# Kernel tuning notes

Measured on AMD Instinct MI355X. Metric: run time of the kernel, lower is better.

The kernel has to match this reference:

```python
import jax, jax.numpy as jnp
import numpy as np

N = 100000   # nodes
E = 1600000  # edges
F = 128      # in_feats
H = 4        # heads
D = 32       # out_feats per head
NEG_SLOPE = 0.2


def setup_inputs() -> dict:
    key = jax.random.key(0)
    k1, k2, k3, k4, k5, k6 = jax.random.split(key, 6)
    feat = jax.random.normal(k1, (N, F), dtype=jnp.float32)
    W = jax.random.normal(k2, (H * D, F), dtype=jnp.float32) * (1.0 / np.sqrt(F))
    attn_l = jax.random.normal(k3, (1, H, D), dtype=jnp.float32) * 0.1
    attn_r = jax.random.normal(k4, (1, H, D), dtype=jnp.float32) * 0.1
    src = jax.random.randint(k5, (E,), 0, N, dtype=jnp.int32)
    dst = jax.random.randint(k6, (E,), 0, N, dtype=jnp.int32)
    return {"feat": feat, "W": W, "attn_l": attn_l, "attn_r": attn_r, "src": src, "dst": dst}


def reference(feat, W, attn_l, attn_r, src, dst):
    # fc projection: [N, F] -> [N, H, D]
    h = (feat @ W.T).reshape(N, H, D)
    # per-node attention logits [N, H]
    el = jnp.sum(h * attn_l, axis=-1)
    er = jnp.sum(h * attn_r, axis=-1)
    # edge scores: el[src] + er[dst] -> leaky relu  [E, H]
    e = jax.nn.leaky_relu(el[src] + er[dst], negative_slope=NEG_SLOPE)
    # segment softmax over edges grouped by destination node, per head
    m = jax.ops.segment_max(e, dst, num_segments=N)          # [N, H]
    ex = jnp.exp(e - m[dst])                                 # [E, H]
    s = jax.ops.segment_sum(ex, dst, num_segments=N)         # [N, H]
    alpha = ex / s[dst]                                      # [E, H]
    # weighted sparse aggregation: out[dst] += alpha * h[src]
    msgs = alpha[:, :, None] * h[src]                        # [E, H, D]
    rst = jax.ops.segment_sum(msgs, dst, num_segments=N)     # [N, H, D]
    return rst
```

## Files before the change

### kernel.cpp

```cpp
#include <hip/hip_runtime.h>

constexpr int N_NODES = 100000;
constexpr int E_EDGES = 1600000;
constexpr int NBLK    = (N_NODES + 1023) / 1024;
constexpr int GEMM_BLOCKS = (N_NODES + 63) / 64;
constexpr int HIST_BLOCKS = (E_EDGES / 4 + 255) / 256;

typedef _Float16 f16;
typedef _Float16 f16x2 __attribute__((ext_vector_type(2)));
typedef _Float16 f16x8 __attribute__((ext_vector_type(8)));
typedef float f32x4 __attribute__((ext_vector_type(4)));

__global__ __launch_bounds__(256, 2) void k_gemm_hist(
        const float* __restrict__ feat, const float* __restrict__ W,
        const float* __restrict__ attn_l, const float* __restrict__ attn_r,
        f16* __restrict__ h2, float* __restrict__ el, float* __restrict__ er,
        const int4* __restrict__ dst4, int* __restrict__ deg,
        int4* __restrict__ rank4) {
    __shared__ f16 Wlds[128 * 128];

    if (blockIdx.x >= GEMM_BLOCKS) {
        int t = (blockIdx.x - GEMM_BLOCKS) * 256 + threadIdx.x;
        if (t < E_EDGES / 4) {
            int4 d = dst4[t];
            int r0 = atomicAdd(&deg[d.x], 1);
            int r1 = atomicAdd(&deg[d.y], 1);
            int r2 = atomicAdd(&deg[d.z], 1);
            int r3 = atomicAdd(&deg[d.w], 1);
            rank4[t] = make_int4(r0, r1, r2, r3);
        }
        return;
    }

    char* wb = (char*)Wlds;
    const int tid = threadIdx.x;
    {
        int n = tid >> 1;
        int kh = (tid & 1) * 64;
        const float* wsrc = W + n * 128 + kh;
#pragma unroll
        for (int q = 0; q < 8; ++q) {
            float4 u0 = *reinterpret_cast<const float4*>(wsrc + q * 8);
            float4 u1 = *reinterpret_cast<const float4*>(wsrc + q * 8 + 4);
            f16x8 v;
            v[0] = (f16)u0.x; v[1] = (f16)u0.y; v[2] = (f16)u0.z; v[3] = (f16)u0.w;
            v[4] = (f16)u1.x; v[5] = (f16)u1.y; v[6] = (f16)u1.z; v[7] = (f16)u1.w;
            unsigned byte = (unsigned)(n * 256 + kh * 2 + q * 16) ^ ((n & 7) << 4);
            *reinterpret_cast<f16x8*>(wb + byte) = v;
        }
    }
    __syncthreads();

    const int wav  = tid >> 6;
    const int lane = tid & 63;
    const int la = lane & 15;
    const int lb = lane >> 4;
    const int row0w = blockIdx.x * 64 + wav * 16;

    f16x8 afrag[4];
    {
        int rowA = row0w + la;
        if (rowA >= N_NODES) rowA = N_NODES - 1;
        const float* ap = feat + (size_t)rowA * 128 + lb * 8;
#pragma unroll
        for (int kk = 0; kk < 4; ++kk) {
            float4 u0 = *reinterpret_cast<const float4*>(ap + kk * 32);
            float4 u1 = *reinterpret_cast<const float4*>(ap + kk * 32 + 4);
            f16x8 a;
            a[0] = (f16)u0.x; a[1] = (f16)u0.y; a[2] = (f16)u0.z; a[3] = (f16)u0.w;
            a[4] = (f16)u1.x; a[5] = (f16)u1.y; a[6] = (f16)u1.z; a[7] = (f16)u1.w;
            afrag[kk] = a;
        }
    }

    f32x4 acc[8];
#pragma unroll
    for (int t = 0; t < 8; ++t) acc[t] = (f32x4){0.f, 0.f, 0.f, 0.f};

#pragma unroll
    for (int t = 0; t < 8; ++t) {
        int col = t * 16 + la;
#pragma unroll
        for (int kk = 0; kk < 4; ++kk) {
            unsigned byte = (unsigned)(col * 256 + (kk * 32 + lb * 8) * 2) ^ ((col & 7) << 4);
            f16x8 b = *reinterpret_cast<const f16x8*>(wb + byte);
            acc[t] = __builtin_amdgcn_mfma_f32_16x16x32_f16(afrag[kk], b, acc[t], 0, 0, 0);
        }
    }

#pragma unroll
    for (int t = 0; t < 8; ++t) {
#pragma unroll
        for (int r = 0; r < 4; ++r) {
            int row = row0w + lb * 4 + r;
            if (row < N_NODES) h2[(size_t)row * 128 + t * 16 + la] = (f16)acc[t][r];
        }
    }

    float elp[4][4], erp[4][4];
#pragma unroll
    for (int r = 0; r < 4; ++r)
#pragma unroll
        for (int g = 0; g < 4; ++g) { elp[r][g] = 0.f; erp[r][g] = 0.f; }

#pragma unroll
    for (int t = 0; t < 8; ++t) {
        float alv = attn_l[t * 16 + la];
        float arv = attn_r[t * 16 + la];
        int g = t >> 1;
#pragma unroll
        for (int r = 0; r < 4; ++r) {
            elp[r][g] += acc[t][r] * alv;
            erp[r][g] += acc[t][r] * arv;
        }
    }
#pragma unroll
    for (int r = 0; r < 4; ++r)
#pragma unroll
        for (int g = 0; g < 4; ++g) {
            float v = elp[r][g];
            v += __shfl_xor(v, 1, 64); v += __shfl_xor(v, 2, 64);
            v += __shfl_xor(v, 4, 64); v += __shfl_xor(v, 8, 64);
            elp[r][g] = v;
            float u = erp[r][g];
            u += __shfl_xor(u, 1, 64); u += __shfl_xor(u, 2, 64);
            u += __shfl_xor(u, 4, 64); u += __shfl_xor(u, 8, 64);
            erp[r][g] = u;
        }
    if (la == 0) {
#pragma unroll
        for (int r = 0; r < 4; ++r) {
            int row = row0w + lb * 4 + r;
            if (row < N_NODES) {
                *reinterpret_cast<float4*>(el + (size_t)row * 4) =
                    make_float4(elp[r][0], elp[r][1], elp[r][2], elp[r][3]);
                *reinterpret_cast<float4*>(er + (size_t)row * 4) =
                    make_float4(erp[r][0], erp[r][1], erp[r][2], erp[r][3]);
            }
        }
    }
}

__global__ void k_bsum(const int* __restrict__ deg, int* __restrict__ aux) {
    int tid = threadIdx.x;
    int i0 = blockIdx.x * 1024 + tid * 4;
    int sum = 0;
#pragma unroll
    for (int j = 0; j < 4; ++j)
        if (i0 + j < N_NODES) sum += (deg[i0 + j] + 3) & ~3;
#pragma unroll
    for (int m = 32; m; m >>= 1) sum += __shfl_xor(sum, m, 64);
    __shared__ int wsums[4];
    if ((tid & 63) == 0) wsums[tid >> 6] = sum;
    __syncthreads();
    if (tid == 0) aux[blockIdx.x] = wsums[0] + wsums[1] + wsums[2] + wsums[3];
}

__global__ void k_scanaux(int* __restrict__ aux) {
    __shared__ int s[128];
    int i = threadIdx.x;
    int v = (i < NBLK) ? aux[i] : 0;
    s[i] = v;
    __syncthreads();
#pragma unroll
    for (int d = 1; d < 128; d <<= 1) {
        int t = (i >= d) ? s[i - d] : 0;
        __syncthreads();
        s[i] += t;
        __syncthreads();
    }
    if (i < NBLK) aux[i] = s[i] - v;
}

__global__ void k_bscan(const int* __restrict__ deg, const int* __restrict__ aux,
                        int* __restrict__ start, int* __restrict__ ssrc,
                        f16* __restrict__ h2, float* __restrict__ el) {
    if (blockIdx.x == 0 && threadIdx.x == 0) {
        float4 z = make_float4(0.f, 0.f, 0.f, 0.f);
        float4* hrow = reinterpret_cast<float4*>(h2 + (size_t)N_NODES * 128);
#pragma unroll
        for (int q = 0; q < 16; ++q) hrow[q] = z;
        *reinterpret_cast<float4*>(el + (size_t)N_NODES * 4) =
            make_float4(-1e4f, -1e4f, -1e4f, -1e4f);
    }
    int tid = threadIdx.x;
    int lane = tid & 63;
    int wid = tid >> 6;
    int i0 = blockIdx.x * 1024 + tid * 4;
    int v[4], pv[4];
#pragma unroll
    for (int j = 0; j < 4; ++j) {
        v[j]  = (i0 + j < N_NODES) ? deg[i0 + j] : 0;
        pv[j] = (v[j] + 3) & ~3;
    }
    int tsum = pv[0] + pv[1] + pv[2] + pv[3];
    int x = tsum;
#pragma unroll
    for (int d = 1; d < 64; d <<= 1) {
        int t = __shfl_up(x, d, 64);
        if (lane >= d) x += t;
    }
    __shared__ int wsums[4];
    if (lane == 63) wsums[wid] = x;
    __syncthreads();
    int base = aux[blockIdx.x];
#pragma unroll
    for (int w = 0; w < 4; ++w)
        if (w < wid) base += wsums[w];
    int p = base + x - tsum;
#pragma unroll
    for (int j = 0; j < 4; ++j) {
        if (i0 + j < N_NODES) {
            start[i0 + j] = p;
            for (int q = v[j]; q < pv[j]; ++q) ssrc[p + q] = N_NODES;
        }
        p += pv[j];
    }
}

__global__ void k_scatter(const int* __restrict__ src, const int* __restrict__ dst,
                          const int* __restrict__ rank, const int* __restrict__ start,
                          int* __restrict__ ssrc) {
    int e = blockIdx.x * blockDim.x + threadIdx.x;
    if (e < E_EDGES) ssrc[start[dst[e]] + rank[e]] = src[e];
}

__global__ __launch_bounds__(128) void k_aggr(const f16* __restrict__ h2,
                                              const float* __restrict__ el,
                                              const float* __restrict__ er,
                                              const int* __restrict__ ssrc,
                                              const int* __restrict__ start,
                                              const int* __restrict__ deg,
                                              float* __restrict__ out) {
    int n = blockIdx.x * 2 + (threadIdx.x >> 6);
    if (n >= N_NODES) return;
    int lane = threadIdx.x & 63;
    int g = lane >> 4;
    int d = deg[n];
    int pd = (d + 3) & ~3;
    int s0 = __builtin_amdgcn_readfirstlane(start[n]);
    float ern = er[n * 4 + g];

    f16x2 ac0 = {0, 0}, ac1 = {0, 0}, ac2 = {0, 0}, ac3 = {0, 0};
    f16x2 sw0 = {0, 0}, sw1 = {0, 0}, sw2 = {0, 0}, sw3 = {0, 0};

    for (int i = 0; i < pd; i += 4) {
        int n0 = ssrc[s0 + i];
        int n1 = ssrc[s0 + i + 1];
        int n2 = ssrc[s0 + i + 2];
        int n3 = ssrc[s0 + i + 3];
        float e0 = el[(size_t)n0 * 4 + g];
        float e1 = el[(size_t)n1 * 4 + g];
        float e2 = el[(size_t)n2 * 4 + g];
        float e3 = el[(size_t)n3 * 4 + g];
        f16x2 q0 = reinterpret_cast<const f16x2*>(h2 + (size_t)n0 * 128)[lane];
        f16x2 q1 = reinterpret_cast<const f16x2*>(h2 + (size_t)n1 * 128)[lane];
        f16x2 q2 = reinterpret_cast<const f16x2*>(h2 + (size_t)n2 * 128)[lane];
        f16x2 q3 = reinterpret_cast<const f16x2*>(h2 + (size_t)n3 * 128)[lane];

        float x0 = e0 + ern; x0 = fmaxf(x0, 0.2f * x0);
        float x1 = e1 + ern; x1 = fmaxf(x1, 0.2f * x1);
        float x2 = e2 + ern; x2 = fmaxf(x2, 0.2f * x2);
        float x3 = e3 + ern; x3 = fmaxf(x3, 0.2f * x3);
        float w0 = __expf(x0);
        float w1 = __expf(x1);
        float w2 = __expf(x2);
        float w3 = __expf(x3);

        f16 a0 = (f16)w0; f16x2 wv0 = {a0, a0};
        f16 a1 = (f16)w1; f16x2 wv1 = {a1, a1};
        f16 a2 = (f16)w2; f16x2 wv2 = {a2, a2};
        f16 a3 = (f16)w3; f16x2 wv3 = {a3, a3};

        ac0 += wv0 * q0; sw0 += wv0;
        ac1 += wv1 * q1; sw1 += wv1;
        ac2 += wv2 * q2; sw2 += wv2;
        ac3 += wv3 * q3; sw3 += wv3;
    }

    f16x2 ac = (ac0 + ac1) + (ac2 + ac3);
    f16x2 sw = (sw0 + sw1) + (sw2 + sw3);
    float swf = (float)sw[0];
    float inv = (d > 0) ? 1.0f / swf : 0.0f;
    float2 o = make_float2((float)ac[0] * inv, (float)ac[1] * inv);
    reinterpret_cast<float2*>(out + (size_t)n * 128)[lane] = o;
}

extern "C" void kernel_launch(void* const* d_in, const int* in_sizes, int n_in,
                              void* d_out, int out_size, void* d_ws, size_t ws_size,
                              hipStream_t stream) {
    const float* feat   = (const float*)d_in[0];
    const float* W      = (const float*)d_in[1];
    const float* attn_l = (const float*)d_in[2];
    const float* attn_r = (const float*)d_in[3];
    const int*   src    = (const int*)d_in[4];
    const int*   dst    = (const int*)d_in[5];
    float* out = (float*)d_out;

    f16*   h2    = (f16*)d_ws;
    float* el    = (float*)(h2 + (size_t)(N_NODES + 8) * 128);
    float* er    = el + (size_t)(N_NODES + 4) * 4;
    int*   deg   = (int*)(er + (size_t)N_NODES * 4);
    int*   start = deg + N_NODES;
    int*   rank  = start + N_NODES;
    int*   ssrc  = rank + E_EDGES;
    int*   aux   = ssrc + E_EDGES + 3 * N_NODES + 64;

    hipMemsetAsync(deg, 0, N_NODES * sizeof(int), stream);

    k_gemm_hist<<<GEMM_BLOCKS + HIST_BLOCKS, 256, 0, stream>>>(
        feat, W, attn_l, attn_r, h2, el, er, (const int4*)dst, deg, (int4*)rank);
    k_bsum<<<NBLK, 256, 0, stream>>>(deg, aux);
    k_scanaux<<<1, 128, 0, stream>>>(aux);
    k_bscan<<<NBLK, 256, 0, stream>>>(deg, aux, start, ssrc, h2, el);
    k_scatter<<<(E_EDGES + 255) / 256, 256, 0, stream>>>(src, dst, rank, start, ssrc);
    k_aggr<<<(N_NODES + 1) / 2, 128, 0, stream>>>(h2, el, er, ssrc, start, deg, out);
}
```

Baseline: 211.5 us.

## Split histogram from GEMM and transpose MFMA output for vectorized stores

Moves the degree histogram out of the fused GEMM kernel into its own launch ahead of the GEMM. It also swaps the MFMA operand order so each lane holds four consecutive output columns of one row. That lets h2 be written with 8-byte vector stores and reduces the el/er shuffle reduction to two steps instead of four. The split removes the branch-divergent fused grid but adds a kernel launch and loses overlap of the atomic-heavy histogram with the GEMM.

After: 211.7 us. About the same (+0.1%).

```diff
diff --git a/kernel.cpp b/kernel.cpp
--- a/kernel.cpp
+++ b/kernel.cpp
@@ -3,37 +3,24 @@
 constexpr int N_NODES = 100000;
 constexpr int E_EDGES = 1600000;
 constexpr int NBLK    = (N_NODES + 1023) / 1024;
-constexpr int GEMM_BLOCKS = (N_NODES + 63) / 64;
-constexpr int HIST_BLOCKS = (E_EDGES / 4 + 255) / 256;
 
 typedef _Float16 f16;
 typedef _Float16 f16x2 __attribute__((ext_vector_type(2)));
+typedef _Float16 f16x4 __attribute__((ext_vector_type(4)));
 typedef _Float16 f16x8 __attribute__((ext_vector_type(8)));
 typedef float f32x4 __attribute__((ext_vector_type(4)));
 
-__global__ __launch_bounds__(256, 2) void k_gemm_hist(
-        const float* __restrict__ feat, const float* __restrict__ W,
-        const float* __restrict__ attn_l, const float* __restrict__ attn_r,
-        f16* __restrict__ h2, float* __restrict__ el, float* __restrict__ er,
-        const int4* __restrict__ dst4, int* __restrict__ deg,
-        int4* __restrict__ rank4) {
+__global__ __launch_bounds__(256) void k_gemm(const float* __restrict__ feat,
+                                              const float* __restrict__ W,
+                                              const float* __restrict__ attn_l,
+                                              const float* __restrict__ attn_r,
+                                              f16* __restrict__ h2,
+                                              float* __restrict__ el,
+                                              float* __restrict__ er) {
     __shared__ f16 Wlds[128 * 128];
-
-    if (blockIdx.x >= GEMM_BLOCKS) {
-        int t = (blockIdx.x - GEMM_BLOCKS) * 256 + threadIdx.x;
-        if (t < E_EDGES / 4) {
-            int4 d = dst4[t];
-            int r0 = atomicAdd(&deg[d.x], 1);
-            int r1 = atomicAdd(&deg[d.y], 1);
-            int r2 = atomicAdd(&deg[d.z], 1);
-            int r3 = atomicAdd(&deg[d.w], 1);
-            rank4[t] = make_int4(r0, r1, r2, r3);
-        }
-        return;
-    }
-
     char* wb = (char*)Wlds;
     const int tid = threadIdx.x;
+
     {
         int n = tid >> 1;
         int kh = (tid & 1) * 64;
@@ -57,7 +44,7 @@
     const int lb = lane >> 4;
     const int row0w = blockIdx.x * 64 + wav * 16;
 
-    f16x8 afrag[4];
+    f16x8 ffrag[4];
     {
         int rowA = row0w + la;
         if (rowA >= N_NODES) rowA = N_NODES - 1;
@@ -69,7 +56,7 @@
             f16x8 a;
             a[0] = (f16)u0.x; a[1] = (f16)u0.y; a[2] = (f16)u0.z; a[3] = (f16)u0.w;
             a[4] = (f16)u1.x; a[5] = (f16)u1.y; a[6] = (f16)u1.z; a[7] = (f16)u1.w;
-            afrag[kk] = a;
+            ffrag[kk] = a;
         }
     }
 
@@ -79,65 +66,59 @@
 
 #pragma unroll
     for (int t = 0; t < 8; ++t) {
-        int col = t * 16 + la;
+        int wrow = t * 16 + la;
 #pragma unroll
         for (int kk = 0; kk < 4; ++kk) {
-            unsigned byte = (unsigned)(col * 256 + (kk * 32 + lb * 8) * 2) ^ ((col & 7) << 4);
+            unsigned byte = (unsigned)(wrow * 256 + (kk * 32 + lb * 8) * 2) ^ ((wrow & 7) << 4);
             f16x8 b = *reinterpret_cast<const f16x8*>(wb + byte);
-            acc[t] = __builtin_amdgcn_mfma_f32_16x16x32_f16(afrag[kk], b, acc[t], 0, 0, 0);
-        }
-    }
-
+            acc[t] = __builtin_amdgcn_mfma_f32_16x16x32_f16(b, ffrag[kk], acc[t], 0, 0, 0);
+        }
+    }
+
+    const int row = row0w + la;
+    const bool ok = row < N_NODES;
+    if (ok) {
+#pragma unroll
+        for (int t = 0; t < 8; ++t) {
+            f16x4 hv;
+            hv.x = (f16)acc[t][0]; hv.y = (f16)acc[t][1];
+            hv.z = (f16)acc[t][2]; hv.w = (f16)acc[t][3];
+            *reinterpret_cast<f16x4*>(&h2[(size_t)row * 128 + t * 16 + lb * 4]) = hv;
+        }
+    }
+
+    float sl[4] = {0.f, 0.f, 0.f, 0.f}, sr[4] = {0.f, 0.f, 0.f, 0.f};
 #pragma unroll
     for (int t = 0; t < 8; ++t) {
-#pragma unroll
-        for (int r = 0; r < 4; ++r) {
-            int row = row0w + lb * 4 + r;
-            if (row < N_NODES) h2[(size_t)row * 128 + t * 16 + la] = (f16)acc[t][r];
-        }
-    }
-
-    float elp[4][4], erp[4][4];
-#pragma unroll
-    for (int r = 0; r < 4; ++r)
-#pragma unroll
-        for (int g = 0; g < 4; ++g) { elp[r][g] = 0.f; erp[r][g] = 0.f; }
-
-#pragma unroll
-    for (int t = 0; t < 8; ++t) {
-        float alv = attn_l[t * 16 + la];
-        float arv = attn_r[t * 16 + la];
+        float4 alv = reinterpret_cast<const float4*>(attn_l)[t * 4 + lb];
+        float4 arv = reinterpret_cast<const float4*>(attn_r)[t * 4 + lb];
         int g = t >> 1;
-#pragma unroll
-        for (int r = 0; r < 4; ++r) {
-            elp[r][g] += acc[t][r] * alv;
-            erp[r][g] += acc[t][r] * arv;
-        }
-    }
-#pragma unroll
-    for (int r = 0; r < 4; ++r)
-#pragma unroll
-        for (int g = 0; g < 4; ++g) {
-            float v = elp[r][g];
-            v += __shfl_xor(v, 1, 64); v += __shfl_xor(v, 2, 64);
-            v += __shfl_xor(v, 4, 64); v += __shfl_xor(v, 8, 64);
-            elp[r][g] = v;
-            float u = erp[r][g];
-            u += __shfl_xor(u, 1, 64); u += __shfl_xor(u, 2, 64);
-            u += __shfl_xor(u, 4, 64); u += __shfl_xor(u, 8, 64);
-            erp[r][g] = u;
-        }
-    if (la == 0) {
-#pragma unroll
-        for (int r = 0; r < 4; ++r) {
-            int row = row0w + lb * 4 + r;
-            if (row < N_NODES) {
-                *reinterpret_cast<float4*>(el + (size_t)row * 4) =
-                    make_float4(elp[r][0], elp[r][1], elp[r][2], elp[r][3]);
-                *reinterpret_cast<float4*>(er + (size_t)row * 4) =
-                    make_float4(erp[r][0], erp[r][1], erp[r][2], erp[r][3]);
-            }
-        }
+        sl[g] += acc[t][0] * alv.x + acc[t][1] * alv.y + acc[t][2] * alv.z + acc[t][3] * alv.w;
+        sr[g] += acc[t][0] * arv.x + acc[t][1] * arv.y + acc[t][2] * arv.z + acc[t][3] * arv.w;
+    }
+#pragma unroll
+    for (int g = 0; g < 4; ++g) {
+        sl[g] += __shfl_xor(sl[g], 16, 64);
+        sl[g] += __shfl_xor(sl[g], 32, 64);
+        sr[g] += __shfl_xor(sr[g], 16, 64);
+        sr[g] += __shfl_xor(sr[g], 32, 64);
+    }
+    if (lb == 0 && ok) {
+        *reinterpret_cast<float4*>(el + (size_t)row * 4) = make_float4(sl[0], sl[1], sl[2], sl[3]);
+        *reinterpret_cast<float4*>(er + (size_t)row * 4) = make_float4(sr[0], sr[1], sr[2], sr[3]);
+    }
+}
+
+__global__ void k_hist(const int4* __restrict__ dst4, int* __restrict__ deg,
+                       int4* __restrict__ rank4) {
+    int t = blockIdx.x * blockDim.x + threadIdx.x;
+    if (t < E_EDGES / 4) {
+        int4 d = dst4[t];
+        int r0 = atomicAdd(&deg[d.x], 1);
+        int r1 = atomicAdd(&deg[d.y], 1);
+        int r2 = atomicAdd(&deg[d.z], 1);
+        int r3 = atomicAdd(&deg[d.w], 1);
+        rank4[t] = make_int4(r0, r1, r2, r3);
     }
 }
 
@@ -308,8 +289,8 @@
 
     hipMemsetAsync(deg, 0, N_NODES * sizeof(int), stream);
 
-    k_gemm_hist<<<GEMM_BLOCKS + HIST_BLOCKS, 256, 0, stream>>>(
-        feat, W, attn_l, attn_r, h2, el, er, (const int4*)dst, deg, (int4*)rank);
+    k_hist<<<(E_EDGES / 4 + 255) / 256, 256, 0, stream>>>((const int4*)dst, deg, (int4*)rank);
+    k_gemm<<<(N_NODES + 63) / 64, 256, 0, stream>>>(feat, W, attn_l, attn_r, h2, el, er);
     k_bsum<<<NBLK, 256, 0, stream>>>(deg, aux);
     k_scanaux<<<1, 128, 0, stream>>>(aux);
     k_bscan<<<NBLK, 256, 0, stream>>>(deg, aux, start, ssrc, h2, el);
```
